# Optimization experiments

Hardware: AMD Instinct MI355X
Metric: run time of the kernel (lower is better)

## Reference

```python
import jax, jax.numpy as jnp
import numpy as np

B = 2
DIMS = ((41, 800, 800), (21, 400, 400), (11, 200, 200), (6, 100, 100))  # (D,H,W)=(z,y,x) per level
VS = ((0.1, 0.1, 0.2), (0.2, 0.2, 0.4), (0.4, 0.4, 0.8), (0.8, 0.8, 1.6))  # (vx,vy,vz)
OFFSET = (0.0, -40.0, -3.0)  # world offset (x,y,z)
BN_EPS = 1e-3

OFFS27 = jnp.array([[z, y, x] for z in (-1, 0, 1) for y in (-1, 0, 1) for x in (-1, 0, 1)], jnp.int32)

# ---------------- numpy-side input construction ----------------

def _np_downsample(coords, out_dims):
    # active output sites of SparseConv3d(k=3, s=2, p=1): in = 2*o - 1 + kd, kd in 0..2
    outs = []
    for kz in range(3):
        for ky in range(3):
            for kx in range(3):
                o = coords[:, 1:] + 1 - np.array([kz, ky, kx])
                ok = (o % 2 == 0).all(1)
                oc = o // 2
                ok &= (oc >= 0).all(1)
                ok &= (oc[:, 0] < out_dims[0]) & (oc[:, 1] < out_dims[1]) & (oc[:, 2] < out_dims[2])
                outs.append(np.concatenate([coords[ok, :1], oc[ok]], 1))
    return np.unique(np.concatenate(outs, 0), axis=0).astype(np.int32)


def _make_coords(rng):
    per_batch = []
    D0, H0, W0 = DIMS[0]
    for b in range(B):
        nc = 120
        centers = np.stack([rng.integers(3, D0 - 4, nc), rng.integers(5, H0 - 6, nc), rng.integers(5, W0 - 6, nc)], 1)
        offs = rng.integers(-3, 4, (nc, 40, 3))
        p = np.clip((centers[:, None, :] + offs).reshape(-1, 3), 0, np.array(DIMS[0]) - 1)
        p = np.unique(p, axis=0)  # sorted lexicographically == sorted by linear key
        per_batch.append(np.concatenate([np.full((len(p), 1), b), p], 1))
    return np.concatenate(per_batch, 0).astype(np.int32)


def setup_inputs():
    rng = np.random.default_rng(0)
    coords0 = _make_coords(rng)
    coords1 = _np_downsample(coords0, DIMS[1])
    coords2 = _np_downsample(coords1, DIMS[2])
    coords3 = _np_downsample(coords2, DIMS[3])
    n = coords0.shape[0]
    c = coords0.astype(np.float64)
    x = OFFSET[0] + (c[:, 3] + 0.5) * VS[0][0] + rng.uniform(-0.04, 0.04, n)
    y = OFFSET[1] + (c[:, 2] + 0.5) * VS[0][1] + rng.uniform(-0.04, 0.04, n)
    z = OFFSET[2] + (c[:, 1] + 0.5) * VS[0][2] + rng.uniform(-0.08, 0.08, n)
    vf = np.stack([x, y, z, rng.uniform(0.0, 1.0, n)], 1).astype(np.float32)

    def conv_w(k, cin, cout):
        return (rng.standard_normal((k, cin, cout)) / np.sqrt(k * cin)).astype(np.float32)

    def bn_p(ch):
        return np.stack([1.0 + 0.05 * rng.standard_normal(ch), 0.05 * rng.standard_normal(ch)], 0).astype(np.float32)

    inp = dict(voxel_features=vf, coords0=coords0, coords1=coords1, coords2=coords2, coords3=coords3,
               w00=conv_w(27, 4, 16), b00=bn_p(16), w01=conv_w(27, 16, 16), b01=bn_p(16),
               wd0=conv_w(27, 16, 32), bd0=bn_p(32),
               w10=conv_w(27, 32, 32), b10=bn_p(32), w11=conv_w(27, 32, 32), b11=bn_p(32),
               wd1=conv_w(27, 32, 64), bd1=bn_p(64),
               w20=conv_w(27, 64, 64), b20=bn_p(64), w21=conv_w(27, 64, 64), b21=bn_p(64), w22=conv_w(27, 64, 64), b22=bn_p(64),
               wd2=conv_w(27, 64, 64), bd2=bn_p(64),
               w30=conv_w(27, 64, 64), b30=bn_p(64), w31=conv_w(27, 64, 64), b31=bn_p(64), w32=conv_w(27, 64, 64), b32=bn_p(64),
               we=(rng.standard_normal((64, 64)) / 8.0).astype(np.float32), be=bn_p(64),
               fc_w=(rng.standard_normal((64, 160)) / np.sqrt(160.0)).astype(np.float32),
               cls_w=(rng.standard_normal((1, 64)) / 8.0).astype(np.float32),
               reg_w=(rng.standard_normal((3, 64)) / 8.0).astype(np.float32))
    return {k: jnp.asarray(v) for k, v in inp.items()}

# ---------------- jax sparse-conv primitives ----------------

def _key(c, dims):
    D, H, W = dims
    return ((c[:, 0] * D + c[:, 1]) * H + c[:, 2]) * W + c[:, 3]


def _gather(nb_b, nb, feats, keys_sorted, dims):
    # nb: (N,27,3) candidate (z,y,x); gather rows of feats via sorted-key lookup, zeros if absent
    D, H, W = dims
    inb = (nb[..., 0] >= 0) & (nb[..., 0] < D) & (nb[..., 1] >= 0) & (nb[..., 1] < H) & (nb[..., 2] >= 0) & (nb[..., 2] < W)
    nbc = jnp.clip(nb, 0, jnp.array(dims, jnp.int32) - 1)
    qk = ((nb_b * D + nbc[..., 0]) * H + nbc[..., 1]) * W + nbc[..., 2]
    pos = jnp.clip(jnp.searchsorted(keys_sorted, qk), 0, keys_sorted.shape[0] - 1)
    found = inb & (keys_sorted[pos] == qk)
    return jnp.where(found[..., None], feats[pos], 0.0)


def _subm(feats, coords, keys, dims, w):
    nb = coords[:, None, 1:] + OFFS27[None]
    g = _gather(coords[:, None, 0], nb, feats, keys, dims)  # (N,27,Cin)
    return jnp.einsum('nkc,kco->no', g, w)


def _stride(feats, in_keys, in_dims, coords_out, w):
    nb = coords_out[:, None, 1:] * 2 + OFFS27[None]  # in = 2*o - 1 + kd
    g = _gather(coords_out[:, None, 0], nb, feats, in_keys, in_dims)
    return jnp.einsum('nkc,kco->no', g, w)


def _bn_relu(x, p):
    # train-mode BatchNorm1d over active voxels (biased var), eps=1e-3
    m = x.mean(0)
    v = jnp.mean((x - m) ** 2, 0)
    return jax.nn.relu((x - m) * jax.lax.rsqrt(v + BN_EPS) * p[0] + p[1])


def _t2p(coords, vs):
    c = coords.astype(jnp.float32)
    x = OFFSET[0] + (c[:, 3] + 0.5) * vs[0]
    y = OFFSET[1] + (c[:, 2] + 0.5) * vs[1]
    z = OFFSET[2] + (c[:, 1] + 0.5) * vs[2]
    return jnp.stack([c[:, 0], x, y, z], 1)


def _nn_interp(unknown, known, feats):
    # three_nn (squared L2, batch-separated, non-differentiable) + three_interpolate
    d2 = jnp.sum((unknown[:, None, 1:] - known[None, :, 1:]) ** 2, -1)
    d2 = d2 + 1e10 * (unknown[:, None, 0] != known[None, :, 0])
    d2 = jax.lax.stop_gradient(d2)
    negd, idx = jax.lax.top_k(-d2, 3)
    w = 1.0 / (-negd + 1e-8)
    w = w / w.sum(1, keepdims=True)
    return jnp.sum(feats[idx] * w[..., None], 1)


def _forward(voxel_features, w00, b00, w01, b01, wd0, bd0, w10, b10, w11, b11, wd1, bd1,
             w20, b20, w21, b21, w22, b22, wd2, bd2, w30, b30, w31, b31, w32, b32,
             we, be, fc_w, cls_w, reg_w, coords0, coords1, coords2, coords3):
    k0, k1 = _key(coords0, DIMS[0]), _key(coords1, DIMS[1])
    k2 = _key(coords2, DIMS[2])
    points_mean = jnp.concatenate([coords0[:, :1].astype(jnp.float32), voxel_features[:, :3]], 1)
    f = _bn_relu(_subm(voxel_features, coords0, k0, DIMS[0], w00), b00)
    f = _bn_relu(_subm(f, coords0, k0, DIMS[0], w01), b01)
    f = _bn_relu(_stride(f, k0, DIMS[0], coords1, wd0), bd0)
    f = _bn_relu(_subm(f, coords1, k1, DIMS[1], w10), b10)
    f = _bn_relu(_subm(f, coords1, k1, DIMS[1], w11), b11)
    p1 = _nn_interp(points_mean, _t2p(coords1, VS[1]), f)
    f = _bn_relu(_stride(f, k1, DIMS[1], coords2, wd1), bd1)
    f = _bn_relu(_subm(f, coords2, k2, DIMS[2], w20), b20)
    f = _bn_relu(_subm(f, coords2, k2, DIMS[2], w21), b21)
    f = _bn_relu(_subm(f, coords2, k2, DIMS[2], w22), b22)
    p2 = _nn_interp(points_mean, _t2p(coords2, VS[2]), f)
    f = _bn_relu(_stride(f, k2, DIMS[2], coords3, wd2), bd2)
    k3 = _key(coords3, DIMS[3])
    f = _bn_relu(_subm(f, coords3, k3, DIMS[3], w30), b30)
    f = _bn_relu(_subm(f, coords3, k3, DIMS[3], w31), b31)
    f = _bn_relu(_subm(f, coords3, k3, DIMS[3], w32), b32)
    p3 = _nn_interp(points_mean, _t2p(coords3, VS[3]), f)
    out = _bn_relu(f @ we, be)  # extra_conv: 1x1x1 SparseConv3d
    D3, H3, W3 = DIMS[3]
    dense = jnp.zeros((B, D3, H3, W3, 64), out.dtype).at[coords3[:, 0], coords3[:, 1], coords3[:, 2], coords3[:, 3]].set(out)
    xd = dense.transpose(0, 4, 1, 2, 3).reshape(B, 64 * D3, H3, W3)  # (N, C*D, H, W)
    pw = jnp.concatenate([p1, p2, p3], 1) @ fc_w.T
    return (xd, points_mean, pw @ cls_w.T, pw @ reg_w.T)


def reference(voxel_features, w00, b00, w01, b01, wd0, bd0, w10, b10, w11, b11, wd1, bd1,
              w20, b20, w21, b21, w22, b22, wd2, bd2, w30, b30, w31, b31, w32, b32,
              we, be, fc_w, cls_w, reg_w, coords0, coords1, coords2, coords3):
    return _forward(voxel_features, w00, b00, w01, b01, wd0, bd0, w10, b10, w11, b11, wd1, bd1,
                    w20, b20, w21, b21, w22, b22, wd2, bd2, w30, b30, w31, b31, w32, b32,
                    we, be, fc_w, cls_w, reg_w, coords0, coords1, coords2, coords3)
```

## Files before the change

kernel.cpp:

```cpp
#include <hip/hip_runtime.h>

#define OFFX 0.0f
#define OFFY -40.0f
#define OFFZ -3.0f
#define BNEPS 1e-3f
#define NCH 128
#define NG 9

typedef _Float16 h2_t __attribute__((ext_vector_type(2)));
__device__ inline h2_t u2h(unsigned u) { union { unsigned u; h2_t h; } x; x.u = u; return x.h; }
__device__ inline unsigned h2u(h2_t h) { union { unsigned u; h2_t h; } x; x.h = h; return x.u; }

__global__ void keys_k(const int* __restrict__ coords, int n, int D, int H, int W,
                       int* __restrict__ keys) {
  int i = blockIdx.x * 256 + threadIdx.x;
  if (i < n) {
    const int* c = coords + (size_t)i * 4;
    keys[i] = ((c[0] * D + c[1]) * H + c[2]) * W + c[3];
  }
}

__global__ void nbr_k(const int* __restrict__ coords, int np, const int* __restrict__ keys, int nk,
                      int D, int H, int W, int scale, int* __restrict__ nbr) {
  int t = blockIdx.x * 256 + threadIdx.x;
  if (t >= np * 27) return;
  int p = t / 27, k = t % 27;
  int kz = k / 9 - 1, ky = (k / 3) % 3 - 1, kx = k % 3 - 1;
  const int* c = coords + (size_t)p * 4;
  int z = c[1] * scale + kz, y = c[2] * scale + ky, x = c[3] * scale + kx;
  int r = -1;
  if (z >= 0 && z < D && y >= 0 && y < H && x >= 0 && x < W) {
    int q = ((c[0] * D + z) * H + y) * W + x;
    int lo = 0, hi = nk;
    while (lo < hi) { int m = (lo + hi) >> 1; if (keys[m] < q) lo = m + 1; else hi = m; }
    if (lo < nk && keys[lo] == q) r = lo;
  }
  nbr[t] = r;
}

struct WPrep { const float* src; unsigned* dst; int cin; int cout; };
struct WP13 { WPrep l[13]; };
__global__ void wprep_k(WP13 a) {
  WPrep w = a.l[blockIdx.y];
  int cp2 = w.cin / 2;
  int tot = 27 * cp2 * w.cout;
  int i = blockIdx.x * 256 + threadIdx.x;
  if (i >= tot) return;
  int o = i % w.cout, rest = i / w.cout;
  int cp = rest % cp2, k = rest / cp2;
  float lo = w.src[((size_t)k * w.cin + 2 * cp) * w.cout + o];
  float hi = w.src[((size_t)k * w.cin + 2 * cp + 1) * w.cout + o];
  h2_t h; h[0] = (_Float16)lo; h[1] = (_Float16)hi;
  w.dst[i] = h2u(h);
}

template<int CIN, int COUT>
__global__ __launch_bounds__(128) void convg_k(const float* __restrict__ feats,
                                               const int* __restrict__ nbr,
                                               const float* __restrict__ w, int n,
                                               float* __restrict__ partial, int gstride) {
  constexpr int TP = 32;
  constexpr int LDP = 36;
  constexpr int CO = COUT / 16;
  __shared__ float G[CIN * LDP];
  int tid = threadIdx.x;
  int pg = tid >> 4, cg = tid & 15;
  int p0 = blockIdx.x * TP;
  int k0 = blockIdx.y * 3;
  float acc[4][CO];
#pragma unroll
  for (int i = 0; i < 4; i++)
#pragma unroll
    for (int j = 0; j < CO; j++) acc[i][j] = 0.f;

  for (int kk = 0; kk < 3; kk++) {
    int k = k0 + kk;
    __syncthreads();
    for (int ch = tid; ch < TP * CIN / 4; ch += 128) {
      int r = ch & (TP - 1), c4 = ch / TP;
      int p = p0 + r;
      int idx = (p < n) ? nbr[(size_t)p * 27 + k] : -1;
      float4 fv = make_float4(0.f, 0.f, 0.f, 0.f);
      if (idx >= 0) fv = *(const float4*)(feats + (size_t)idx * CIN + c4 * 4);
      G[(c4 * 4 + 0) * LDP + r] = fv.x;
      G[(c4 * 4 + 1) * LDP + r] = fv.y;
      G[(c4 * 4 + 2) * LDP + r] = fv.z;
      G[(c4 * 4 + 3) * LDP + r] = fv.w;
    }
    __syncthreads();
    const float* wk = w + (size_t)k * CIN * COUT + cg * CO;
#pragma unroll
    for (int c = 0; c < CIN; c++) {
      float4 g4 = *(const float4*)&G[c * LDP + pg * 4];
      float wv[CO];
      if constexpr (CO == 4)      *(float4*)wv = *(const float4*)(wk + c * COUT);
      else if constexpr (CO == 2) *(float2*)wv = *(const float2*)(wk + c * COUT);
      else                        wv[0] = wk[c * COUT];
      float gp[4] = {g4.x, g4.y, g4.z, g4.w};
#pragma unroll
      for (int i = 0; i < 4; i++)
#pragma unroll
        for (int j = 0; j < CO; j++) acc[i][j] = fmaf(gp[i], wv[j], acc[i][j]);
    }
  }
#pragma unroll
  for (int i = 0; i < 4; i++) {
    int p = p0 + pg * 4 + i;
    if (p < n) {
      float* dst = partial + (size_t)blockIdx.y * gstride + (size_t)p * COUT + cg * CO;
      if constexpr (CO == 4)      *(float4*)dst = *(float4*)acc[i];
      else if constexpr (CO == 2) *(float2*)dst = *(float2*)acc[i];
      else                        dst[0] = acc[i][0];
    }
  }
}

template<int CIN, int COUT>
__global__ __launch_bounds__(128) void convh_k(const unsigned* __restrict__ fh,
                                               const int* __restrict__ nbr,
                                               const unsigned* __restrict__ wh, int n,
                                               float* __restrict__ partial, int gstride,
                                               const float* __restrict__ scsh) {
  constexpr int TP = 32;
  constexpr int LDPH = 36;
  constexpr int CO = COUT / 16;
  constexpr int CP = CIN / 2;
  __shared__ unsigned H[CP * LDPH];
  int tid = threadIdx.x;
  int pg = tid >> 4, cg = tid & 15;
  int p0 = blockIdx.x * TP;
  int k0 = blockIdx.y * 3;
  int r = tid & 31;
  int p = p0 + r;
  int sidx[3];
  if (p < n) {
    const int* nb = nbr + (size_t)p * 27 + k0;
    sidx[0] = nb[0]; sidx[1] = nb[1]; sidx[2] = nb[2];
  } else { sidx[0] = sidx[1] = sidx[2] = -1; }

  float acc[4][CO];
#pragma unroll
  for (int i = 0; i < 4; i++)
#pragma unroll
    for (int j = 0; j < CO; j++) acc[i][j] = 0.f;

  if constexpr (CIN >= 32) {
    constexpr int NLD = CIN / 32;
    uint4 pf[NLD];
    {
      int idx = sidx[0];
#pragma unroll
      for (int it = 0; it < NLD; it++) {
        int q = (tid >> 5) + it * 4;
        pf[it] = (idx >= 0) ? *(const uint4*)(fh + (size_t)idx * CP + q * 4)
                            : make_uint4(0, 0, 0, 0);
      }
    }
    for (int kk = 0; kk < 3; kk++) {
      bool ok = sidx[kk] >= 0;
      __syncthreads();
#pragma unroll
      for (int it = 0; it < NLD; it++) {
        int q = (tid >> 5) + it * 4;
        unsigned uu[4] = {pf[it].x, pf[it].y, pf[it].z, pf[it].w};
#pragma unroll
        for (int j = 0; j < 4; j++) {
          int cp = q * 4 + j;
          unsigned outw = 0;
          if (ok) {
            h2_t h = u2h(uu[j]);
            float lo = fmaxf(fmaf((float)h[0], scsh[2 * cp], scsh[CIN + 2 * cp]), 0.f);
            float hi = fmaxf(fmaf((float)h[1], scsh[2 * cp + 1], scsh[CIN + 2 * cp + 1]), 0.f);
            h2_t o; o[0] = (_Float16)lo; o[1] = (_Float16)hi;
            outw = h2u(o);
          }
          H[cp * LDPH + r] = outw;
        }
      }
      if (kk < 2) {
        int idx = sidx[kk + 1];
#pragma unroll
        for (int it = 0; it < NLD; it++) {
          int q = (tid >> 5) + it * 4;
          pf[it] = (idx >= 0) ? *(const uint4*)(fh + (size_t)idx * CP + q * 4)
                              : make_uint4(0, 0, 0, 0);
        }
      }
      __syncthreads();
      const unsigned* wk = wh + (size_t)(k0 + kk) * CP * COUT + cg * CO;
#pragma unroll 8
      for (int cp = 0; cp < CP; cp++) {
        uint4 g4 = *(const uint4*)&H[cp * LDPH + pg * 4];
        unsigned gg[4] = {g4.x, g4.y, g4.z, g4.w};
        unsigned wv[CO];
        if constexpr (CO == 4)      *(uint4*)wv = *(const uint4*)(wk + cp * COUT);
        else if constexpr (CO == 2) *(uint2*)wv = *(const uint2*)(wk + cp * COUT);
        else                        wv[0] = wk[cp * COUT];
#pragma unroll
        for (int i = 0; i < 4; i++)
#pragma unroll
          for (int j = 0; j < CO; j++)
            acc[i][j] = __builtin_amdgcn_fdot2(u2h(gg[i]), u2h(wv[j]), acc[i][j], false);
      }
    }
  } else {
    int q = tid >> 5;
    uint2 pf2;
    {
      int idx = sidx[0];
      pf2 = (idx >= 0) ? *(const uint2*)(fh + (size_t)idx * CP + q * 2) : make_uint2(0, 0);
    }
    for (int kk = 0; kk < 3; kk++) {
      bool ok = sidx[kk] >= 0;
      __syncthreads();
      unsigned uu[2] = {pf2.x, pf2.y};
#pragma unroll
      for (int j = 0; j < 2; j++) {
        int cp = q * 2 + j;
        unsigned outw = 0;
        if (ok) {
          h2_t h = u2h(uu[j]);
          float lo = fmaxf(fmaf((float)h[0], scsh[2 * cp], scsh[CIN + 2 * cp]), 0.f);
          float hi = fmaxf(fmaf((float)h[1], scsh[2 * cp + 1], scsh[CIN + 2 * cp + 1]), 0.f);
          h2_t o; o[0] = (_Float16)lo; o[1] = (_Float16)hi;
          outw = h2u(o);
        }
        H[cp * LDPH + r] = outw;
      }
      if (kk < 2) {
        int idx = sidx[kk + 1];
        pf2 = (idx >= 0) ? *(const uint2*)(fh + (size_t)idx * CP + q * 2) : make_uint2(0, 0);
      }
      __syncthreads();
      const unsigned* wk = wh + (size_t)(k0 + kk) * CP * COUT + cg * CO;
#pragma unroll
      for (int cp = 0; cp < CP; cp++) {
        uint4 g4 = *(const uint4*)&H[cp * LDPH + pg * 4];
        unsigned gg[4] = {g4.x, g4.y, g4.z, g4.w};
        unsigned wv[CO];
        if constexpr (CO == 4)      *(uint4*)wv = *(const uint4*)(wk + cp * COUT);
        else if constexpr (CO == 2) *(uint2*)wv = *(const uint2*)(wk + cp * COUT);
        else                        wv[0] = wk[cp * COUT];
#pragma unroll
        for (int i = 0; i < 4; i++)
#pragma unroll
          for (int j = 0; j < CO; j++)
            acc[i][j] = __builtin_amdgcn_fdot2(u2h(gg[i]), u2h(wv[j]), acc[i][j], false);
      }
    }
  }
#pragma unroll
  for (int i = 0; i < 4; i++) {
    int pp = p0 + pg * 4 + i;
    if (pp < n) {
      float* dst = partial + (size_t)blockIdx.y * gstride + (size_t)pp * COUT + cg * CO;
      if constexpr (CO == 4)      *(float4*)dst = *(float4*)acc[i];
      else if constexpr (CO == 2) *(float2*)dst = *(float2*)acc[i];
      else                        dst[0] = acc[i][0];
    }
  }
}

__global__ void bn_k(const float* __restrict__ partial, int G, int gstride, int n, int C,
                     float* __restrict__ pre, unsigned* __restrict__ preh,
                     float* __restrict__ stats, const float* __restrict__ bnp,
                     float* __restrict__ scsh, int* __restrict__ ctr) {
  __shared__ float l1e[256], l2e[256], l1o[256], l2o[256];
  __shared__ int lastf;
  int t = threadIdx.x;
  int total = n * C;
  float s1e = 0.f, s2e = 0.f, s1o = 0.f, s2o = 0.f;
  for (int i2 = (blockIdx.x * 256 + t) * 2; i2 < total; i2 += NCH * 512) {
    float v0 = 0.f, v1 = 0.f;
    for (int g = 0; g < G; g++) {
      float2 pv = *(const float2*)(partial + (size_t)g * gstride + i2);
      v0 += pv.x; v1 += pv.y;
    }
    if (pre) *(float2*)(pre + i2) = make_float2(v0, v1);
    h2_t h; h[0] = (_Float16)v0; h[1] = (_Float16)v1;
    preh[i2 >> 1] = h2u(h);
    s1e += v0; s2e += v0 * v0; s1o += v1; s2o += v1 * v1;
  }
  l1e[t] = s1e; l2e[t] = s2e; l1o[t] = s1o; l2o[t] = s2o;
  for (int s = 128; s >= C / 2; s >>= 1) {
    __syncthreads();
    if (t < s) {
      l1e[t] += l1e[t + s]; l2e[t] += l2e[t + s];
      l1o[t] += l1o[t + s]; l2o[t] += l2o[t + s];
    }
  }
  __syncthreads();
  if (t < C / 2) {
    stats[((size_t)blockIdx.x * C + 2 * t) * 2]     = l1e[t];
    stats[((size_t)blockIdx.x * C + 2 * t) * 2 + 1] = l2e[t];
    stats[((size_t)blockIdx.x * C + 2 * t + 1) * 2]     = l1o[t];
    stats[((size_t)blockIdx.x * C + 2 * t + 1) * 2 + 1] = l2o[t];
  }
  __threadfence();
  __syncthreads();
  if (t == 0) lastf = (atomicAdd(ctr, 1) == NCH - 1) ? 1 : 0;
  __syncthreads();
  if (lastf) {
    __threadfence();
    if (t < C) {
      float a1 = 0.f, a2 = 0.f;
      for (int ch = 0; ch < NCH; ch++) {
        a1 += stats[((size_t)ch * C + t) * 2];
        a2 += stats[((size_t)ch * C + t) * 2 + 1];
      }
      float m = a1 / n;
      float v = a2 / n - m * m;
      float sc = bnp[t] / sqrtf(v + BNEPS);
      scsh[t] = sc;
      scsh[C + t] = bnp[C + t] - m * sc;
    }
  }
}

__global__ void pm_k(const float* __restrict__ vf, const int* __restrict__ c0, int n0,
                     float* __restrict__ pm, float* __restrict__ out1) {
  int i = blockIdx.x * 256 + threadIdx.x;
  if (i >= n0) return;
  float b = (float)c0[(size_t)i * 4];
  float x = vf[(size_t)i * 4], y = vf[(size_t)i * 4 + 1], z = vf[(size_t)i * 4 + 2];
  pm[(size_t)i * 4] = b; pm[(size_t)i * 4 + 1] = x; pm[(size_t)i * 4 + 2] = y; pm[(size_t)i * 4 + 3] = z;
  out1[(size_t)i * 4] = b; out1[(size_t)i * 4 + 1] = x; out1[(size_t)i * 4 + 2] = y; out1[(size_t)i * 4 + 3] = z;
}

__global__ void knnprep_k(const int* __restrict__ coords, int nl, float vx, float vy, float vz,
                          float4* __restrict__ kp4, int* __restrict__ bs) {
  int i = blockIdx.x * 256 + threadIdx.x;
  if (i >= nl) return;
  const int* c = coords + (size_t)i * 4;
  kp4[i] = make_float4(OFFX + (c[3] + 0.5f) * vx,
                       OFFY + (c[2] + 0.5f) * vy,
                       OFFZ + (c[1] + 0.5f) * vz, (float)c[0]);
  if (c[0] == 0 && (i + 1 == nl || coords[(size_t)(i + 1) * 4] == 1)) bs[0] = i + 1;
}

__global__ __launch_bounds__(256) void knn_k(const float4* __restrict__ pm4, int n0,
                                             const float4* __restrict__ kp4, int nl,
                                             const int* __restrict__ bsp,
                                             float* __restrict__ wv, int* __restrict__ iv) {
  __shared__ __align__(16) float4 kp[256];
  __shared__ int bl[4], bh[4];
  int tid = threadIdx.x;
  int wave = tid >> 6, lane = tid & 63;
  int u = blockIdx.x * 4 + wave;
  bool valid = u < n0;
  float4 up = pm4[valid ? u : (n0 - 1)];
  int bs = bsp[0];
  int lo = (up.x == 0.f) ? 0 : bs;
  int hi = (up.x == 0.f) ? bs : nl;
  if (!valid) { lo = 0; hi = 0; }
  if (lane == 0) { bl[wave] = valid ? lo : 0x7fffffff; bh[wave] = valid ? hi : 0; }
  __syncthreads();
  int blo = min(min(bl[0], bl[1]), min(bl[2], bl[3]));
  int bhi = max(max(bh[0], bh[1]), max(bh[2], bh[3]));
  float ux = up.y, uy = up.z, uz = up.w;
  float d0 = 3e38f, d1 = 3e38f, d2 = 3e38f;
  int i0 = -1, i1 = -1, i2 = -1;
#define INS1(DD, GI) { \
    bool l0 = (DD) < d0, l1 = (DD) < d1, l2 = (DD) < d2; \
    i2 = l2 ? (l1 ? i1 : (GI)) : i2; \
    i1 = l1 ? (l0 ? i0 : (GI)) : i1; \
    i0 = l0 ? (GI) : i0; \
    float t1_ = __builtin_amdgcn_fmed3f(d0, d1, (DD)); \
    float t2_ = __builtin_amdgcn_fmed3f(d1, d2, (DD)); \
    d0 = fminf(d0, (DD)); d1 = t1_; d2 = t2_; }
#define DIST(Q) fmaf(ux - (Q).x, ux - (Q).x, fmaf(uy - (Q).y, uy - (Q).y, (uz - (Q).z) * (uz - (Q).z)))
  for (int cb = blo; cb < bhi; cb += 256) {
    int m = bhi - cb; if (m > 256) m = 256;
    __syncthreads();
    if (tid < m) kp[tid] = kp4[cb + tid];
    __syncthreads();
    if (cb + 256 <= lo || cb >= hi) continue;
    if (m == 256 && cb >= lo && cb + 256 <= hi) {
      float4 q0 = kp[lane], q1 = kp[lane + 64], q2 = kp[lane + 128], q3 = kp[lane + 192];
      float a0 = DIST(q0), a1 = DIST(q1), a2 = DIST(q2), a3 = DIST(q3);
      INS1(a0, cb + lane) INS1(a1, cb + lane + 64) INS1(a2, cb + lane + 128) INS1(a3, cb + lane + 192)
    } else {
#pragma unroll
      for (int j = 0; j < 4; j++) {
        int i = lane + 64 * j;
        int e = cb + i;
        if (i < m && e >= lo && e < hi) {
          float4 q = kp[i];
          float dd = DIST(q);
          INS1(dd, e)
        }
      }
    }
  }
#pragma unroll
  for (int off = 1; off < 64; off <<= 1) {
    float e0 = __shfl_xor(d0, off), e1 = __shfl_xor(d1, off), e2 = __shfl_xor(d2, off);
    int j0 = __shfl_xor(i0, off), j1 = __shfl_xor(i1, off), j2 = __shfl_xor(i2, off);
    INS1(e0, j0) INS1(e1, j1) INS1(e2, j2)
  }
#undef DIST
#undef INS1
  if (valid && lane == 0) {
    float w0 = 1.f / (d0 + 1e-8f), w1 = 1.f / (d1 + 1e-8f), w2 = 1.f / (d2 + 1e-8f);
    float s = w0 + w1 + w2;
    wv[(size_t)u * 3] = w0 / s; wv[(size_t)u * 3 + 1] = w1 / s; wv[(size_t)u * 3 + 2] = w2 / s;
    iv[(size_t)u * 3] = i0; iv[(size_t)u * 3 + 1] = i1; iv[(size_t)u * 3 + 2] = i2;
  }
}

__global__ void interp_k(const unsigned* __restrict__ fh, int C, const float* __restrict__ scsh,
                         const float* __restrict__ wv, const int* __restrict__ iv, int n0,
                         float* __restrict__ X, int xoff) {
  int t = blockIdx.x * 256 + threadIdx.x;
  if (t >= n0 * C) return;
  int u = t / C, c = t % C;
  int cp = c >> 1, sel = c & 1;
  int CP = C >> 1;
  float sc = scsh[c], sh = scsh[C + c];
  h2_t h0 = u2h(fh[(size_t)iv[(size_t)u * 3]     * CP + cp]);
  h2_t h1 = u2h(fh[(size_t)iv[(size_t)u * 3 + 1] * CP + cp]);
  h2_t h2v = u2h(fh[(size_t)iv[(size_t)u * 3 + 2] * CP + cp]);
  float a0 = fmaxf(fmaf((float)h0[sel], sc, sh), 0.f);
  float a1 = fmaxf(fmaf((float)h1[sel], sc, sh), 0.f);
  float a2 = fmaxf(fmaf((float)h2v[sel], sc, sh), 0.f);
  X[(size_t)u * 160 + xoff + c] = wv[(size_t)u * 3] * a0 + wv[(size_t)u * 3 + 1] * a1
                                + wv[(size_t)u * 3 + 2] * a2;
}

__global__ __launch_bounds__(256) void conv1x1_k(const unsigned* __restrict__ fh,
                                                 const float* __restrict__ scsh,
                                                 const float* __restrict__ we, int n,
                                                 float* __restrict__ out) {
  __shared__ float rows[256];
  int t = threadIdx.x;
  int p = blockIdx.x * 4 + (t >> 6), c = t & 63;
  float v = 0.f;
  if (p < n) {
    h2_t h = u2h(fh[(size_t)p * 32 + (c >> 1)]);
    v = fmaxf(fmaf((float)h[c & 1], scsh[c], scsh[64 + c]), 0.f);
  }
  rows[t] = v;
  __syncthreads();
  if (p >= n) return;
  const float* fr = rows + (t >> 6) * 64;
  float a = 0.f;
#pragma unroll 16
  for (int ci = 0; ci < 64; ci++) a = fmaf(fr[ci], we[ci * 64 + c], a);
  out[(size_t)p * 64 + c] = a;
}

__global__ void scatter_k(const float* __restrict__ pre, const float* __restrict__ scsh,
                          const int* __restrict__ c3, int n3, float* __restrict__ out0) {
  int t = blockIdx.x * 256 + threadIdx.x;
  if (t >= n3 * 64) return;
  int p = t >> 6, c = t & 63;
  const int* cc = c3 + (size_t)p * 4;
  size_t o = ((((size_t)cc[0] * 64 + c) * 6 + cc[1]) * 100 + cc[2]) * 100 + cc[3];
  out0[o] = fmaxf(fmaf(pre[t], scsh[c], scsh[64 + c]), 0.f);
}

__global__ __launch_bounds__(256) void head_k(const float* __restrict__ X,
                                              const float* __restrict__ fcw,
                                              const float* __restrict__ clsw,
                                              const float* __restrict__ regw,
                                              int n0, float* __restrict__ outc,
                                              float* __restrict__ outr) {
  __shared__ float fl[64 * 161];
  int t = threadIdx.x;
  for (int i = t; i < 64 * 160; i += 256) {
    int r = i / 160, c = i % 160;
    fl[r * 161 + c] = fcw[i];
  }
  __syncthreads();
  int wave = t >> 6, lane = t & 63;
  int u = blockIdx.x * 4 + wave;
  if (u >= n0) return;
  const float* xr = X + (size_t)u * 160;
  const float* wr = fl + (size_t)lane * 161;
  float a = 0.f;
#pragma unroll 8
  for (int i = 0; i < 160; i++) a = fmaf(xr[i], wr[i], a);
  float c = a * clsw[lane];
  float r0 = a * regw[lane], r1 = a * regw[64 + lane], r2 = a * regw[128 + lane];
  for (int off = 32; off; off >>= 1) {
    c  += __shfl_down(c, off);
    r0 += __shfl_down(r0, off);
    r1 += __shfl_down(r1, off);
    r2 += __shfl_down(r2, off);
  }
  if (lane == 0) {
    outc[u] = c;
    outr[(size_t)u * 3] = r0; outr[(size_t)u * 3 + 1] = r1; outr[(size_t)u * 3 + 2] = r2;
  }
}

extern "C" void kernel_launch(void* const* d_in, const int* in_sizes, int n_in,
                              void* d_out, int out_size, void* d_ws, size_t ws_size,
                              hipStream_t stream) {
  const float* vf  = (const float*)d_in[0];
  const int* c0 = (const int*)d_in[1];
  const int* c1 = (const int*)d_in[2];
  const int* c2 = (const int*)d_in[3];
  const int* c3 = (const int*)d_in[4];
  const float* w00 = (const float*)d_in[5];  const float* b00 = (const float*)d_in[6];
  const float* w01 = (const float*)d_in[7];  const float* b01 = (const float*)d_in[8];
  const float* wd0 = (const float*)d_in[9];  const float* bd0 = (const float*)d_in[10];
  const float* w10 = (const float*)d_in[11]; const float* b10 = (const float*)d_in[12];
  const float* w11 = (const float*)d_in[13]; const float* b11 = (const float*)d_in[14];
  const float* wd1 = (const float*)d_in[15]; const float* bd1 = (const float*)d_in[16];
  const float* w20 = (const float*)d_in[17]; const float* b20 = (const float*)d_in[18];
  const float* w21 = (const float*)d_in[19]; const float* b21 = (const float*)d_in[20];
  const float* w22 = (const float*)d_in[21]; const float* b22 = (const float*)d_in[22];
  const float* wd2 = (const float*)d_in[23]; const float* bd2 = (const float*)d_in[24];
  const float* w30 = (const float*)d_in[25]; const float* b30 = (const float*)d_in[26];
  const float* w31 = (const float*)d_in[27]; const float* b31 = (const float*)d_in[28];
  const float* w32 = (const float*)d_in[29]; const float* b32 = (const float*)d_in[30];
  const float* we  = (const float*)d_in[31]; const float* be  = (const float*)d_in[32];
  const float* fcw = (const float*)d_in[33];
  const float* clsw = (const float*)d_in[34];
  const float* regw = (const float*)d_in[35];

  int N0 = in_sizes[1] / 4, N1 = in_sizes[2] / 4, N2 = in_sizes[3] / 4, N3 = in_sizes[4] / 4;
  int maxN = N0; if (N1 > maxN) maxN = N1; if (N2 > maxN) maxN = N2; if (N3 > maxN) maxN = N3;

  auto cdiv = [](int a, int b) { return (a + b - 1) / b; };
  char* p = (char*)d_ws;
  auto alloc = [&](size_t bytes) { char* r = p; p += (bytes + 255) & ~(size_t)255; return r; };

  int* keys0 = (int*)alloc((size_t)N0 * 4);
  int* keys1 = (int*)alloc((size_t)N1 * 4);
  int* keys2 = (int*)alloc((size_t)N2 * 4);
  int* keys3 = (int*)alloc((size_t)N3 * 4);
  int* nbr0  = (int*)alloc((size_t)N0 * 27 * 4);
  int* nbrs1 = (int*)alloc((size_t)N1 * 27 * 4);
  int* nbr1  = (int*)alloc((size_t)N1 * 27 * 4);
  int* nbrs2 = (int*)alloc((size_t)N2 * 27 * 4);
  int* nbr2  = (int*)alloc((size_t)N2 * 27 * 4);
  int* nbrs3 = (int*)alloc((size_t)N3 * 27 * 4);
  int* nbr3  = (int*)alloc((size_t)N3 * 27 * 4);
  float* FA = (float*)alloc((size_t)maxN * 64 * 4);
  float* FB = (float*)alloc((size_t)maxN * 64 * 4);
  float* FC = (float*)alloc((size_t)maxN * 64 * 4);
  unsigned* FAh = (unsigned*)alloc((size_t)maxN * 32 * 4);
  unsigned* FBh = (unsigned*)alloc((size_t)maxN * 32 * 4);
  float* stats = (float*)alloc((size_t)NCH * 64 * 2 * 4);
  float* SC = (float*)alloc((size_t)15 * 128 * 4);
  int* ctrs = (int*)alloc(16 * 4);
  float* wv = (float*)alloc((size_t)N0 * 3 * 4);
  int*   iv = (int*)alloc((size_t)N0 * 3 * 4);
  float* X  = (float*)alloc((size_t)N0 * 160 * 4);
  float* pmb = (float*)alloc((size_t)N0 * 4 * 4);
  float4* kp1 = (float4*)alloc((size_t)N1 * 16);
  float4* kp2 = (float4*)alloc((size_t)N2 * 16);
  float4* kp3 = (float4*)alloc((size_t)N3 * 16);
  int* bsA = (int*)alloc(32);
  unsigned* whbuf = (unsigned*)alloc((size_t)452736 * 4);

  float* out0 = (float*)d_out;
  float* out1 = out0 + 7680000;
  float* outc = out1 + (size_t)N0 * 4;
  float* outr = outc + N0;
  float* partial = out0;

  auto scsh = [&](int L) { return SC + (size_t)L * 128; };

  const float* wsrc[13] = {w01, wd0, w10, w11, wd1, w20, w21, w22, wd2, w30, w31, w32, nullptr};
  int wcin[13]  = {16, 16, 32, 32, 32, 64, 64, 64, 64, 64, 64, 64, 0};
  int wcout[13] = {16, 32, 32, 32, 64, 64, 64, 64, 64, 64, 64, 64, 0};
  unsigned* wdst[13];
  size_t woff = 0;
  WP13 wp{};
  int nw = 12;
  for (int i = 0; i < nw; i++) {
    wdst[i] = whbuf + woff;
    wp.l[i] = WPrep{wsrc[i], wdst[i], wcin[i], wcout[i]};
    woff += (size_t)27 * (wcin[i] / 2) * wcout[i];
  }
  for (int i = nw; i < 13; i++) wp.l[i] = WPrep{w01, wdst[0], 16, 16};

  hipMemsetAsync(ctrs, 0, 16 * 4, stream);
  wprep_k<<<dim3(216, nw), 256, 0, stream>>>(wp);
  keys_k<<<cdiv(N0, 256), 256, 0, stream>>>(c0, N0, 41, 800, 800, keys0);
  keys_k<<<cdiv(N1, 256), 256, 0, stream>>>(c1, N1, 21, 400, 400, keys1);
  keys_k<<<cdiv(N2, 256), 256, 0, stream>>>(c2, N2, 11, 200, 200, keys2);
  keys_k<<<cdiv(N3, 256), 256, 0, stream>>>(c3, N3, 6, 100, 100, keys3);
  nbr_k<<<cdiv(N0 * 27, 256), 256, 0, stream>>>(c0, N0, keys0, N0, 41, 800, 800, 1, nbr0);
  nbr_k<<<cdiv(N1 * 27, 256), 256, 0, stream>>>(c1, N1, keys0, N0, 41, 800, 800, 2, nbrs1);
  nbr_k<<<cdiv(N1 * 27, 256), 256, 0, stream>>>(c1, N1, keys1, N1, 21, 400, 400, 1, nbr1);
  nbr_k<<<cdiv(N2 * 27, 256), 256, 0, stream>>>(c2, N2, keys1, N1, 21, 400, 400, 2, nbrs2);
  nbr_k<<<cdiv(N2 * 27, 256), 256, 0, stream>>>(c2, N2, keys2, N2, 11, 200, 200, 1, nbr2);
  nbr_k<<<cdiv(N3 * 27, 256), 256, 0, stream>>>(c3, N3, keys2, N2, 11, 200, 200, 2, nbrs3);
  nbr_k<<<cdiv(N3 * 27, 256), 256, 0, stream>>>(c3, N3, keys3, N3, 6, 100, 100, 1, nbr3);
  pm_k<<<cdiv(N0, 256), 256, 0, stream>>>(vf, c0, N0, pmb, out1);
  knnprep_k<<<cdiv(N1, 256), 256, 0, stream>>>(c1, N1, 0.2f, 0.2f, 0.4f, kp1, bsA + 0);
  knnprep_k<<<cdiv(N2, 256), 256, 0, stream>>>(c2, N2, 0.4f, 0.4f, 0.8f, kp2, bsA + 1);
  knnprep_k<<<cdiv(N3, 256), 256, 0, stream>>>(c3, N3, 0.8f, 0.8f, 1.6f, kp3, bsA + 2);

  auto convh = [&](const unsigned* fhin, const int* nb, int wi, int n, int cin, int cout,
                   const float* ss) {
    dim3 g(cdiv(n, 32), NG);
    int gs = n * cout;
    const unsigned* wh = wdst[wi];
    if (cin == 16 && cout == 16)
      convh_k<16, 16><<<g, 128, 0, stream>>>(fhin, nb, wh, n, partial, gs, ss);
    else if (cin == 16 && cout == 32)
      convh_k<16, 32><<<g, 128, 0, stream>>>(fhin, nb, wh, n, partial, gs, ss);
    else if (cin == 32 && cout == 32)
      convh_k<32, 32><<<g, 128, 0, stream>>>(fhin, nb, wh, n, partial, gs, ss);
    else if (cin == 32 && cout == 64)
      convh_k<32, 64><<<g, 128, 0, stream>>>(fhin, nb, wh, n, partial, gs, ss);
    else
      convh_k<64, 64><<<g, 128, 0, stream>>>(fhin, nb, wh, n, partial, gs, ss);
  };
  auto bnp = [&](const float* bnpar, int n, int C, float* pre, unsigned* preh, int L) {
    bn_k<<<NCH, 256, 0, stream>>>(partial, NG, n * C, n, C, pre, preh, stats, bnpar,
                                  scsh(L), ctrs + L);
  };
  auto knn = [&](const float4* kp4, const int* bsl, int nl, const unsigned* fh, int C, int L,
                 int xoff) {
    knn_k<<<cdiv(N0, 4), 256, 0, stream>>>((const float4*)pmb, N0, kp4, nl, bsl, wv, iv);
    interp_k<<<cdiv(N0 * C, 256), 256, 0, stream>>>(fh, C, scsh(L), wv, iv, N0, X, xoff);
  };

  convg_k<4, 16><<<dim3(cdiv(N0, 32), NG), 128, 0, stream>>>(vf, nbr0, w00, N0, partial, N0 * 16);
  bnp(b00, N0, 16, nullptr, FAh, 0);
  convh(FAh, nbr0, 0, N0, 16, 16, scsh(0));   bnp(b01, N0, 16, nullptr, FBh, 1);
  convh(FBh, nbrs1, 1, N1, 16, 32, scsh(1));  bnp(bd0, N1, 32, nullptr, FAh, 2);
  convh(FAh, nbr1, 2, N1, 32, 32, scsh(2));   bnp(b10, N1, 32, nullptr, FBh, 3);
  convh(FBh, nbr1, 3, N1, 32, 32, scsh(3));   bnp(b11, N1, 32, nullptr, FAh, 4);
  knn(kp1, bsA + 0, N1, FAh, 32, 4, 0);
  convh(FAh, nbrs2, 4, N2, 32, 64, scsh(4));  bnp(bd1, N2, 64, nullptr, FBh, 5);
  convh(FBh, nbr2, 5, N2, 64, 64, scsh(5));   bnp(b20, N2, 64, nullptr, FAh, 6);
  convh(FAh, nbr2, 6, N2, 64, 64, scsh(6));   bnp(b21, N2, 64, nullptr, FBh, 7);
  convh(FBh, nbr2, 7, N2, 64, 64, scsh(7));   bnp(b22, N2, 64, nullptr, FAh, 8);
  knn(kp2, bsA + 1, N2, FAh, 64, 8, 32);
  convh(FAh, nbrs3, 8, N3, 64, 64, scsh(8));  bnp(bd2, N3, 64, nullptr, FBh, 9);
  convh(FBh, nbr3, 9, N3, 64, 64, scsh(9));   bnp(b30, N3, 64, nullptr, FAh, 10);
  convh(FAh, nbr3, 10, N3, 64, 64, scsh(10)); bnp(b31, N3, 64, nullptr, FBh, 11);
  convh(FBh, nbr3, 11, N3, 64, 64, scsh(11)); bnp(b32, N3, 64, nullptr, FAh, 12);
  knn(kp3, bsA + 2, N3, FAh, 64, 12, 96);

  conv1x1_k<<<cdiv(N3, 4), 256, 0, stream>>>(FAh, scsh(12), we, N3, FC);
  bn_k<<<NCH, 256, 0, stream>>>(FC, 1, 0, N3, 64, FB, FBh, stats, be, scsh(13), ctrs + 13);
  hipMemsetAsync(d_out, 0, (size_t)7680000 * 4, stream);
  scatter_k<<<cdiv(N3 * 64, 256), 256, 0, stream>>>(FB, scsh(13), c3, N3, out0);
  head_k<<<cdiv(N0, 4), 256, 0, stream>>>(X, fcw, clsw, regw, N0, outc, outr);
}
```

Baseline: 932.0 us.

## Prune KNN candidate chunks with z-sorted seeding and distance bounds

The KNN kernel now first finds, for each query wave, the chunk of z-sorted voxel centers whose z range brackets the query's z, and processes those seed chunks first. It then visits the remaining chunks and skips any whose z-interval distance already exceeds the wave's current best third-nearest bound. Chunks are loaded into shared memory only when at least one wave in the block still needs them. This aims to cut most of the brute-force distance work and shared-memory loads. In exchange it adds ballot scans, extra global reads of chunk endpoints, more block-wide barriers, and a dependence on coordinates being sorted by z within each batch.

```diff
diff --git a/kernel.cpp b/kernel.cpp
--- a/kernel.cpp
+++ b/kernel.cpp
@@ -343,7 +343,7 @@
                                              const int* __restrict__ bsp,
                                              float* __restrict__ wv, int* __restrict__ iv) {
   __shared__ __align__(16) float4 kp[256];
-  __shared__ int bl[4], bh[4];
+  __shared__ int bl[4], bh[4], sseed[4], sflag[4];
   int tid = threadIdx.x;
   int wave = tid >> 6, lane = tid & 63;
   int u = blockIdx.x * 4 + wave;
@@ -360,6 +360,27 @@
   float ux = up.y, uy = up.z, uz = up.w;
   float d0 = 3e38f, d1 = 3e38f, d2 = 3e38f;
   int i0 = -1, i1 = -1, i2 = -1;
+  int NT = (bhi > blo) ? ((bhi - blo + 255) >> 8) : 0;
+
+  int pref = -1;
+  if (valid) {
+    int tfirst = (lo - blo) >> 8;
+    int tlast = (hi - 1 - blo) >> 8;
+    pref = tfirst;
+    for (int base = tfirst + 1; base <= tlast; base += 64) {
+      int t2 = base + lane;
+      bool okf = false;
+      if (t2 <= tlast) {
+        int cs = blo + (t2 << 8);
+        okf = (kp4[cs].z <= uz);
+      }
+      unsigned long long mask = __ballot(okf);
+      if (mask) pref = base + (63 - __builtin_clzll(mask));
+    }
+  }
+  if (lane == 0) sseed[wave] = pref;
+  __syncthreads();
+
 #define INS1(DD, GI) { \
     bool l0 = (DD) < d0, l1 = (DD) < d1, l2 = (DD) < d2; \
     i2 = l2 ? (l1 ? i1 : (GI)) : i2; \
@@ -369,35 +390,71 @@
     float t2_ = __builtin_amdgcn_fmed3f(d1, d2, (DD)); \
     d0 = fminf(d0, (DD)); d1 = t1_; d2 = t2_; }
 #define DIST(Q) fmaf(ux - (Q).x, ux - (Q).x, fmaf(uy - (Q).y, uy - (Q).y, (uz - (Q).z) * (uz - (Q).z)))
-  for (int cb = blo; cb < bhi; cb += 256) {
+#define PROC_CHUNK(CB, M) { \
+    if (!((CB) + 256 <= lo || (CB) >= hi)) { \
+      if ((M) == 256 && (CB) >= lo && (CB) + 256 <= hi) { \
+        float4 q0 = kp[lane], q1 = kp[lane + 64], q2 = kp[lane + 128], q3 = kp[lane + 192]; \
+        float a0 = DIST(q0), a1 = DIST(q1), a2 = DIST(q2), a3 = DIST(q3); \
+        INS1(a0, (CB) + lane) INS1(a1, (CB) + lane + 64) \
+        INS1(a2, (CB) + lane + 128) INS1(a3, (CB) + lane + 192) \
+      } else { \
+        for (int j = 0; j < 4; j++) { \
+          int ii = lane + 64 * j; \
+          int e = (CB) + ii; \
+          if (ii < (M) && e >= lo && e < hi) { \
+            float4 q = kp[ii]; \
+            float dd = DIST(q); \
+            INS1(dd, e) \
+          } \
+        } \
+      } \
+    } }
+
+  for (int w = 0; w < 4; w++) {
+    int t2 = sseed[w];
+    bool skip = (t2 < 0);
+    for (int w2 = 0; w2 < w; w2++) if (sseed[w2] == t2) skip = true;
+    if (skip) continue;
+    int cb = blo + (t2 << 8);
     int m = bhi - cb; if (m > 256) m = 256;
     __syncthreads();
     if (tid < m) kp[tid] = kp4[cb + tid];
     __syncthreads();
-    if (cb + 256 <= lo || cb >= hi) continue;
-    if (m == 256 && cb >= lo && cb + 256 <= hi) {
-      float4 q0 = kp[lane], q1 = kp[lane + 64], q2 = kp[lane + 128], q3 = kp[lane + 192];
-      float a0 = DIST(q0), a1 = DIST(q1), a2 = DIST(q2), a3 = DIST(q3);
-      INS1(a0, cb + lane) INS1(a1, cb + lane + 64) INS1(a2, cb + lane + 128) INS1(a3, cb + lane + 192)
-    } else {
-#pragma unroll
-      for (int j = 0; j < 4; j++) {
-        int i = lane + 64 * j;
-        int e = cb + i;
-        if (i < m && e >= lo && e < hi) {
-          float4 q = kp[i];
-          float dd = DIST(q);
-          INS1(dd, e)
-        }
-      }
-    }
-  }
+    PROC_CHUNK(cb, m)
+  }
+
+  for (int t2 = 0; t2 < NT; t2++) {
+    if (t2 == sseed[0] || t2 == sseed[1] || t2 == sseed[2] || t2 == sseed[3]) continue;
+    int cb = blo + (t2 << 8);
+    int m = bhi - cb; if (m > 256) m = 256;
+    bool skipw = true;
+    int s0 = cb > lo ? cb : lo;
+    int s1 = (cb + m < hi) ? cb + m : hi;
+    if (valid && s0 < s1) {
+      float zl = kp4[s0].z;
+      float zh = kp4[s1 - 1].z;
+      float dz = (uz < zl) ? (zl - uz) : ((uz > zh) ? (uz - zh) : 0.f);
+      float wb = d2;
+#pragma unroll
+      for (int off = 32; off; off >>= 1) wb = fminf(wb, __shfl_xor(wb, off));
+      skipw = (dz * dz > wb);
+    }
+    if (lane == 0) sflag[wave] = skipw ? 1 : 0;
+    __syncthreads();
+    bool allskip = sflag[0] && sflag[1] && sflag[2] && sflag[3];
+    if (!allskip) { if (tid < m) kp[tid] = kp4[cb + tid]; }
+    __syncthreads();
+    if (allskip || skipw) continue;
+    PROC_CHUNK(cb, m)
+  }
+
 #pragma unroll
   for (int off = 1; off < 64; off <<= 1) {
     float e0 = __shfl_xor(d0, off), e1 = __shfl_xor(d1, off), e2 = __shfl_xor(d2, off);
     int j0 = __shfl_xor(i0, off), j1 = __shfl_xor(i1, off), j2 = __shfl_xor(i2, off);
     INS1(e0, j0) INS1(e1, j1) INS1(e2, j2)
   }
+#undef PROC_CHUNK
 #undef DIST
 #undef INS1
   if (valid && lane == 0) {
```

After: 983.8 us. 5.6% more time.
